# Optimization experiments

Measured on AMD Instinct MI355X. Metric: run time of the kernel, lower is better.

## Reference

```python
import jax, jax.numpy as jnp
import numpy as np

N_NODES = 50000

def gcn_conv(x, W, b, src, dst, n):
    # PyG GCNConv: h = x @ W; add self-loops; sym-normalized mean aggregation; + bias
    h = x @ W  # [N, out]
    deg = jax.ops.segment_sum(jnp.ones(src.shape[0], x.dtype), dst, num_segments=n) + 1.0  # +1 self-loop
    dinv = jax.lax.rsqrt(deg)  # deg^{-1/2}
    norm = dinv[src] * dinv[dst]  # [E]
    msg = h[src] * norm[:, None]  # [E, out]
    agg = jax.ops.segment_sum(msg, dst, num_segments=n)
    agg = agg + h * (dinv * dinv)[:, None]  # self-loop contribution, norm = 1/deg
    return agg + b


def setup_inputs() -> dict:
    key = jax.random.key(0)
    ks = jax.random.split(key, 12)
    f1, h1, h2, a = 128, 128, 64, N_NODES
    def glorot(k, shape):
        lim = float(np.sqrt(6.0 / (shape[0] + shape[1])))
        return jax.random.uniform(k, shape, jnp.float32, -lim, lim)
    x = jax.random.normal(ks[0], (N_NODES, f1), jnp.float32)
    edge_index = jax.random.randint(ks[1], (2, 800000), 0, N_NODES, dtype=jnp.int64)
    W1 = glorot(ks[2], (f1, h1)); b1 = jnp.zeros((h1,), jnp.float32)
    W2 = glorot(ks[3], (h1, h2)); b2 = jnp.zeros((h2,), jnp.float32)
    W3 = glorot(ks[4], (h2, 1));  b3 = jnp.zeros((1,), jnp.float32)
    lim4 = float(1.0 / np.sqrt(a))
    W4 = jax.random.uniform(ks[5], (a,), jnp.float32, -lim4, lim4)
    b4 = jax.random.uniform(ks[6], (1,), jnp.float32, -lim4, lim4)
    return {"x": x, "edge_index": edge_index, "W1": W1, "b1": b1,
            "W2": W2, "b2": b2, "W3": W3, "b3": b3, "W4": W4, "b4": b4}


def reference(x, edge_index, W1, b1, W2, b2, W3, b3, W4, b4):
    src, dst = edge_index[0], edge_index[1]
    n = x.shape[0]
    h = jnp.tanh(gcn_conv(x, W1, b1, src, dst, n))
    h = jnp.tanh(gcn_conv(h, W2, b2, src, dst, n))
    h = jnp.tanh(gcn_conv(h, W3, b3, src, dst, n))
    h = h.reshape(-1)  # [N] == action_dim
    out = jnp.dot(W4, h) + b4  # Linear(action_dim, 1) -> [1]
    return out
```

## Files before the change

kernel.cpp:

```cpp
#include <hip/hip_runtime.h>
#include <hip/hip_fp16.h>
#include <math.h>


constexpr int BLOCK = 256;
constexpr int SLOTS = 64;

__device__ inline unsigned int pack_h2(float a, float b) {
    __half2 h = __floats2half2_rn(a, b);
    return *reinterpret_cast<unsigned int*>(&h);
}
__device__ inline float2 unpack_h2(unsigned int u) {
    __half2 h = *reinterpret_cast<__half2*>(&u);
    return __half22float2(h);
}

template<int K, int M>
__global__ void __launch_bounds__(256) gemm1_fill(const float* __restrict__ X,
                                                  const float* __restrict__ W,
                                                  __half* __restrict__ H, int N, int ngemm,
                                                  const int* __restrict__ src,
                                                  const int* __restrict__ dst,
                                                  int* __restrict__ deg,
                                                  unsigned short* __restrict__ slots,
                                                  int E, int nfill) {
    __shared__ float xs[64][64];
    const int rem = blockIdx.x % 3;
    if (rem != 0) {
        int blk = (blockIdx.x / 3) * 2 + (rem - 1);
        if (blk >= nfill) return;
        int base = (blk * blockDim.x + threadIdx.x) * 2;
        if (base + 2 <= E) {
            int2 da = *reinterpret_cast<const int2*>(dst + base);
            int2 sa = *reinterpret_cast<const int2*>(src + base);
            int p0 = atomicAdd(&deg[da.x], 1);
            int p1 = atomicAdd(&deg[da.y], 1);
            if (p0 < SLOTS) slots[(size_t)da.x * SLOTS + p0] = (unsigned short)sa.x;
            if (p1 < SLOTS) slots[(size_t)da.y * SLOTS + p1] = (unsigned short)sa.y;
        } else {
            for (int e = base; e < E; ++e) {
                int d = dst[e];
                int p = atomicAdd(&deg[d], 1);
                if (p < SLOTS) slots[(size_t)d * SLOTS + p] = (unsigned short)src[e];
            }
        }
        return;
    }
    constexpr int BM = 64;
    constexpr int TN = 4;
    constexpr int TX = M / TN;
    constexpr int TY = 256 / TX;
    constexpr int TM = BM / TY;
    constexpr int KH4 = 16;

    int gblk = blockIdx.x / 3;
    if (gblk >= ngemm) return;
    const int tid = threadIdx.x;
    const int n0 = gblk * BM;

    if (gblk == 0 && tid < 32)
        reinterpret_cast<uint2*>(H + (size_t)N * M)[tid] = make_uint2(0u, 0u);

    const int tx = tid % TX;
    const int ty = tid / TX;
    const int col0 = tx * TN;
    const int row0 = ty * TM;

    float acc[TM][TN];
#pragma unroll
    for (int r = 0; r < TM; ++r)
#pragma unroll
        for (int c = 0; c < TN; ++c) acc[r][c] = 0.0f;

    const float4* X4 = reinterpret_cast<const float4*>(X);
    const float4* W4 = reinterpret_cast<const float4*>(W);
    constexpr int X4_PER_ROW = K / 4;
    constexpr int W4_PER_ROW = M / 4;

#pragma unroll
    for (int ph = 0; ph < 2; ++ph) {
#pragma unroll
        for (int i = 0; i < 4; ++i) {
            int idx = tid + i * 256;
            int row = idx >> 4;
            int k4 = idx & 15;
            float4 v = make_float4(0.f, 0.f, 0.f, 0.f);
            if (n0 + row < N) v = X4[(size_t)(n0 + row) * X4_PER_ROW + ph * KH4 + k4];
            *reinterpret_cast<float4*>(&xs[row][k4 * 4]) = v;
        }
        __syncthreads();
#pragma unroll 4
        for (int k4 = 0; k4 < KH4; ++k4) {
            int k4g = ph * KH4 + k4;
            float4 wv[4];
#pragma unroll
            for (int i = 0; i < 4; ++i)
                wv[i] = W4[(size_t)(k4g * 4 + i) * W4_PER_ROW + tx];
            float4 xv[TM];
#pragma unroll
            for (int r = 0; r < TM; ++r)
                xv[r] = *reinterpret_cast<const float4*>(&xs[row0 + r][k4 * 4]);
#pragma unroll
            for (int r = 0; r < TM; ++r) {
#pragma unroll
                for (int c = 0; c < TN; ++c) {
                    acc[r][c] = fmaf(xv[r].x, ((float*)&wv[0])[c], acc[r][c]);
                    acc[r][c] = fmaf(xv[r].y, ((float*)&wv[1])[c], acc[r][c]);
                    acc[r][c] = fmaf(xv[r].z, ((float*)&wv[2])[c], acc[r][c]);
                    acc[r][c] = fmaf(xv[r].w, ((float*)&wv[3])[c], acc[r][c]);
                }
            }
        }
        __syncthreads();
    }

#pragma unroll
    for (int r = 0; r < TM; ++r) {
        int row = n0 + row0 + r;
        if (row < N) {
            uint2 o;
            o.x = pack_h2(acc[r][0], acc[r][1]);
            o.y = pack_h2(acc[r][2], acc[r][3]);
            *reinterpret_cast<uint2*>(&H[(size_t)row * M + col0]) = o;
        }
    }
}

__global__ void dinv_scale(const int* __restrict__ deg, int* __restrict__ cnt,
                           float* __restrict__ dinv, uint2* __restrict__ Hh, int N) {
    int idx = blockIdx.x * blockDim.x + threadIdx.x;
    int n = idx >> 5, q = idx & 31;
    if (n > N) return;
    if (n == N) { if (q == 0) dinv[N] = 0.0f; return; }
    int dg = deg[n];
    float di = 1.0f / sqrtf((float)dg + 1.0f);
    if (q == 0) { dinv[n] = di; cnt[n] = min(dg, SLOTS); }
    uint2 u = Hh[idx];
    float2 a = unpack_h2(u.x);
    float2 b = unpack_h2(u.y);
    uint2 o;
    o.x = pack_h2(a.x * di, a.y * di);
    o.y = pack_h2(b.x * di, b.y * di);
    Hh[idx] = o;
}

template<int K, int M>
__global__ void __launch_bounds__(256) gemm_tiled(const float* __restrict__ X,
                                                  const float* __restrict__ W,
                                                  const float* __restrict__ dinv,
                                                  __half* __restrict__ H, int N) {
    constexpr int BM = 64;
    constexpr int TN = 4;
    constexpr int TX = M / TN;
    constexpr int TY = 256 / TX;
    constexpr int TM = BM / TY;
    constexpr int K4 = K / 4;

    __shared__ float xs[BM][K];

    const int tid = threadIdx.x;
    const int n0 = blockIdx.x * BM;

    if (blockIdx.x == 0 && tid < 16)
        reinterpret_cast<uint2*>(H + (size_t)N * M)[tid] = make_uint2(0u, 0u);

    {
        const float4* X4 = reinterpret_cast<const float4*>(X);
        constexpr int F4_PER_ROW = K / 4;
        constexpr int TOT = BM * F4_PER_ROW;
#pragma unroll
        for (int i = 0; i < TOT / 256; ++i) {
            int idx = tid + i * 256;
            int row = idx / F4_PER_ROW;
            int k4 = idx % F4_PER_ROW;
            float4 v = make_float4(0.f, 0.f, 0.f, 0.f);
            if (n0 + row < N) v = X4[(size_t)(n0 + row) * F4_PER_ROW + k4];
            *reinterpret_cast<float4*>(&xs[row][k4 * 4]) = v;
        }
    }
    __syncthreads();

    const int tx = tid % TX;
    const int ty = tid / TX;
    const int col0 = tx * TN;
    const int row0 = ty * TM;

    float acc[TM][TN];
#pragma unroll
    for (int r = 0; r < TM; ++r)
#pragma unroll
        for (int c = 0; c < TN; ++c) acc[r][c] = 0.0f;

    const float4* W4 = reinterpret_cast<const float4*>(W);
    constexpr int W4_PER_ROW = M / 4;

#pragma unroll 4
    for (int k4 = 0; k4 < K4; ++k4) {
        float4 wv[4];
#pragma unroll
        for (int i = 0; i < 4; ++i)
            wv[i] = W4[(size_t)(k4 * 4 + i) * W4_PER_ROW + tx];
        float4 xv[TM];
#pragma unroll
        for (int r = 0; r < TM; ++r)
            xv[r] = *reinterpret_cast<const float4*>(&xs[row0 + r][k4 * 4]);
#pragma unroll
        for (int r = 0; r < TM; ++r) {
#pragma unroll
            for (int c = 0; c < TN; ++c) {
                acc[r][c] = fmaf(xv[r].x, ((float*)&wv[0])[c], acc[r][c]);
                acc[r][c] = fmaf(xv[r].y, ((float*)&wv[1])[c], acc[r][c]);
                acc[r][c] = fmaf(xv[r].z, ((float*)&wv[2])[c], acc[r][c]);
                acc[r][c] = fmaf(xv[r].w, ((float*)&wv[3])[c], acc[r][c]);
            }
        }
    }

#pragma unroll
    for (int r = 0; r < TM; ++r) {
        int row = n0 + row0 + r;
        if (row < N) {
            float di = dinv[row];
            uint2 o;
            o.x = pack_h2(acc[r][0] * di, acc[r][1] * di);
            o.y = pack_h2(acc[r][2] * di, acc[r][3] * di);
            *reinterpret_cast<uint2*>(&H[(size_t)row * M + col0]) = o;
        }
    }
}

__global__ void __launch_bounds__(256) agg128(const int* __restrict__ cntA,
                                              const unsigned short* __restrict__ slots,
                                              const float* __restrict__ dinv,
                                              const __half* __restrict__ Hs,
                                              const float* __restrict__ bias,
                                              float* __restrict__ A, int N) {
    int wid = threadIdx.x >> 6;
    int lane = threadIdx.x & 63;
    int n = blockIdx.x * 4 + wid;
    if (n >= N) return;
    int half = lane >> 5, sub = lane & 31;
    const uint2* H2 = reinterpret_cast<const uint2*>(Hs);
    float4 acc = make_float4(0.f, 0.f, 0.f, 0.f);
    if (half == 0) {
        uint2 u = H2[(size_t)n * 32 + sub];
        float2 a = unpack_h2(u.x), b = unpack_h2(u.y);
        acc.x = a.x; acc.y = a.y; acc.z = b.x; acc.w = b.y;
    }
    int cnt = cntA[n];
    int idxv = (lane < cnt) ? (int)slots[(size_t)n * SLOTS + lane] : N;
    int cnt16 = (cnt + 15) & ~15;
    for (int j = 0; j < cnt16; j += 16) {
        int s0 = __shfl(idxv, j + half);
        int s1 = __shfl(idxv, j + 2 + half);
        int s2 = __shfl(idxv, j + 4 + half);
        int s3 = __shfl(idxv, j + 6 + half);
        int s4 = __shfl(idxv, j + 8 + half);
        int s5 = __shfl(idxv, j + 10 + half);
        int s6 = __shfl(idxv, j + 12 + half);
        int s7 = __shfl(idxv, j + 14 + half);
        uint2 u0 = H2[(size_t)s0 * 32 + sub];
        uint2 u1 = H2[(size_t)s1 * 32 + sub];
        uint2 u2 = H2[(size_t)s2 * 32 + sub];
        uint2 u3 = H2[(size_t)s3 * 32 + sub];
        uint2 u4 = H2[(size_t)s4 * 32 + sub];
        uint2 u5 = H2[(size_t)s5 * 32 + sub];
        uint2 u6 = H2[(size_t)s6 * 32 + sub];
        uint2 u7 = H2[(size_t)s7 * 32 + sub];
        float2 a0 = unpack_h2(u0.x), b0 = unpack_h2(u0.y);
        float2 a1 = unpack_h2(u1.x), b1 = unpack_h2(u1.y);
        float2 a2 = unpack_h2(u2.x), b2 = unpack_h2(u2.y);
        float2 a3 = unpack_h2(u3.x), b3 = unpack_h2(u3.y);
        float2 a4 = unpack_h2(u4.x), b4 = unpack_h2(u4.y);
        float2 a5 = unpack_h2(u5.x), b5 = unpack_h2(u5.y);
        float2 a6 = unpack_h2(u6.x), b6 = unpack_h2(u6.y);
        float2 a7 = unpack_h2(u7.x), b7 = unpack_h2(u7.y);
        acc.x += (a0.x + a1.x) + (a2.x + a3.x) + (a4.x + a5.x) + (a6.x + a7.x);
        acc.y += (a0.y + a1.y) + (a2.y + a3.y) + (a4.y + a5.y) + (a6.y + a7.y);
        acc.z += (b0.x + b1.x) + (b2.x + b3.x) + (b4.x + b5.x) + (b6.x + b7.x);
        acc.w += (b0.y + b1.y) + (b2.y + b3.y) + (b4.y + b5.y) + (b6.y + b7.y);
    }
    acc.x += __shfl_down(acc.x, 32);
    acc.y += __shfl_down(acc.y, 32);
    acc.z += __shfl_down(acc.z, 32);
    acc.w += __shfl_down(acc.w, 32);
    if (half == 0) {
        float di = dinv[n];
        float4 b = reinterpret_cast<const float4*>(bias)[sub];
        float4 o;
        o.x = tanhf(acc.x * di + b.x);
        o.y = tanhf(acc.y * di + b.y);
        o.z = tanhf(acc.z * di + b.z);
        o.w = tanhf(acc.w * di + b.w);
        reinterpret_cast<float4*>(A)[(size_t)n * 32 + sub] = o;
    }
}

__global__ void __launch_bounds__(256) agg64_dot3(const int* __restrict__ cntA,
                                                  const unsigned short* __restrict__ slots,
                                                  const float* __restrict__ dinv,
                                                  const __half* __restrict__ Hs,
                                                  const float* __restrict__ b2,
                                                  const float* __restrict__ W3,
                                                  float* __restrict__ Hs3, int N) {
    int wid = threadIdx.x >> 6;
    int lane = threadIdx.x & 63;
    int n = blockIdx.x * 4 + wid;
    if (n >= N) return;
    int grp = lane >> 4, sub = lane & 15;
    const uint2* H2 = reinterpret_cast<const uint2*>(Hs);
    float4 acc = make_float4(0.f, 0.f, 0.f, 0.f);
    if (grp == 0) {
        uint2 u = H2[(size_t)n * 16 + sub];
        float2 a = unpack_h2(u.x), b = unpack_h2(u.y);
        acc.x = a.x; acc.y = a.y; acc.z = b.x; acc.w = b.y;
    }
    int cnt = cntA[n];
    int idxv = (lane < cnt) ? (int)slots[(size_t)n * SLOTS + lane] : N;
    int cnt16 = (cnt + 15) & ~15;
    int j = 0;
    for (; j + 32 <= cnt16; j += 32) {
        int s0 = __shfl(idxv, j + grp);
        int s1 = __shfl(idxv, j + 4 + grp);
        int s2 = __shfl(idxv, j + 8 + grp);
        int s3 = __shfl(idxv, j + 12 + grp);
        int s4 = __shfl(idxv, j + 16 + grp);
        int s5 = __shfl(idxv, j + 20 + grp);
        int s6 = __shfl(idxv, j + 24 + grp);
        int s7 = __shfl(idxv, j + 28 + grp);
        uint2 u0 = H2[(size_t)s0 * 16 + sub];
        uint2 u1 = H2[(size_t)s1 * 16 + sub];
        uint2 u2 = H2[(size_t)s2 * 16 + sub];
        uint2 u3 = H2[(size_t)s3 * 16 + sub];
        uint2 u4 = H2[(size_t)s4 * 16 + sub];
        uint2 u5 = H2[(size_t)s5 * 16 + sub];
        uint2 u6 = H2[(size_t)s6 * 16 + sub];
        uint2 u7 = H2[(size_t)s7 * 16 + sub];
        float2 a0 = unpack_h2(u0.x), b0 = unpack_h2(u0.y);
        float2 a1 = unpack_h2(u1.x), b1 = unpack_h2(u1.y);
        float2 a2 = unpack_h2(u2.x), b2f = unpack_h2(u2.y);
        float2 a3 = unpack_h2(u3.x), b3f = unpack_h2(u3.y);
        float2 a4 = unpack_h2(u4.x), b4f = unpack_h2(u4.y);
        float2 a5 = unpack_h2(u5.x), b5f = unpack_h2(u5.y);
        float2 a6 = unpack_h2(u6.x), b6f = unpack_h2(u6.y);
        float2 a7 = unpack_h2(u7.x), b7f = unpack_h2(u7.y);
        acc.x += (a0.x + a1.x) + (a2.x + a3.x) + (a4.x + a5.x) + (a6.x + a7.x);
        acc.y += (a0.y + a1.y) + (a2.y + a3.y) + (a4.y + a5.y) + (a6.y + a7.y);
        acc.z += (b0.x + b1.x) + (b2f.x + b3f.x) + (b4f.x + b5f.x) + (b6f.x + b7f.x);
        acc.w += (b0.y + b1.y) + (b2f.y + b3f.y) + (b4f.y + b5f.y) + (b6f.y + b7f.y);
    }
    for (; j < cnt16; j += 16) {
        int s0 = __shfl(idxv, j + grp);
        int s1 = __shfl(idxv, j + 4 + grp);
        int s2 = __shfl(idxv, j + 8 + grp);
        int s3 = __shfl(idxv, j + 12 + grp);
        uint2 u0 = H2[(size_t)s0 * 16 + sub];
        uint2 u1 = H2[(size_t)s1 * 16 + sub];
        uint2 u2 = H2[(size_t)s2 * 16 + sub];
        uint2 u3 = H2[(size_t)s3 * 16 + sub];
        float2 a0 = unpack_h2(u0.x), b0 = unpack_h2(u0.y);
        float2 a1 = unpack_h2(u1.x), b1 = unpack_h2(u1.y);
        float2 a2 = unpack_h2(u2.x), b2f = unpack_h2(u2.y);
        float2 a3 = unpack_h2(u3.x), b3f = unpack_h2(u3.y);
        acc.x += (a0.x + a1.x) + (a2.x + a3.x);
        acc.y += (a0.y + a1.y) + (a2.y + a3.y);
        acc.z += (b0.x + b1.x) + (b2f.x + b3f.x);
        acc.w += (b0.y + b1.y) + (b2f.y + b3f.y);
    }
    acc.x += __shfl_xor(acc.x, 16);
    acc.y += __shfl_xor(acc.y, 16);
    acc.z += __shfl_xor(acc.z, 16);
    acc.w += __shfl_xor(acc.w, 16);
    acc.x += __shfl_xor(acc.x, 32);
    acc.y += __shfl_xor(acc.y, 32);
    acc.z += __shfl_xor(acc.z, 32);
    acc.w += __shfl_xor(acc.w, 32);
    float di = dinv[n];
    float4 b = reinterpret_cast<const float4*>(b2)[sub];
    float4 w = reinterpret_cast<const float4*>(W3)[sub];
    float t = tanhf(acc.x * di + b.x) * w.x
            + tanhf(acc.y * di + b.y) * w.y
            + tanhf(acc.z * di + b.z) * w.z
            + tanhf(acc.w * di + b.w) * w.w;
#pragma unroll
    for (int off = 1; off < 16; off <<= 1) t += __shfl_xor(t, off);
    if (lane == 0) Hs3[n] = t * di;
}

__global__ void __launch_bounds__(256) agg_dot(const int* __restrict__ cntA,
                                               const unsigned short* __restrict__ slots,
                                               const float* __restrict__ dinv,
                                               const float* __restrict__ Hs,
                                               const float* __restrict__ b3,
                                               const float* __restrict__ W4,
                                               float* __restrict__ partials, int N) {
    __shared__ float sm[4];
    int wid = threadIdx.x >> 6;
    int lane = threadIdx.x & 63;
    int n = blockIdx.x * 4 + wid;
    float p = 0.0f;
    if (n < N) {
        int cnt = cntA[n];
        float acc = (lane < cnt) ? Hs[(int)slots[(size_t)n * SLOTS + lane]] : 0.0f;
#pragma unroll
        for (int off = 32; off > 0; off >>= 1) acc += __shfl_down(acc, off);
        if (lane == 0) {
            float h = tanhf((acc + Hs[n]) * dinv[n] + b3[0]);
            p = W4[n] * h;
        }
    }
    if (lane == 0) sm[wid] = p;
    __syncthreads();
    if (threadIdx.x == 0) partials[blockIdx.x] = sm[0] + sm[1] + sm[2] + sm[3];
}

__global__ void final_sum(const float* __restrict__ partials, int B,
                          const float* __restrict__ b4, float* __restrict__ out) {
    float acc = 0.0f;
    for (int i = threadIdx.x; i < B; i += blockDim.x) acc += partials[i];
#pragma unroll
    for (int off = 32; off > 0; off >>= 1) acc += __shfl_down(acc, off);
    __shared__ float sm[4];
    int lane = threadIdx.x & 63, wid = threadIdx.x >> 6;
    if (lane == 0) sm[wid] = acc;
    __syncthreads();
    if (threadIdx.x == 0) out[0] = sm[0] + sm[1] + sm[2] + sm[3] + b4[0];
}

extern "C" void kernel_launch(void* const* d_in, const int* in_sizes, int n_in,
                              void* d_out, int out_size, void* d_ws, size_t ws_size,
                              hipStream_t stream) {
    const float* x  = (const float*)d_in[0];
    const int*   ei = (const int*)d_in[1];
    const float* W1 = (const float*)d_in[2];
    const float* b1 = (const float*)d_in[3];
    const float* W2 = (const float*)d_in[4];
    const float* b2 = (const float*)d_in[5];
    const float* W3 = (const float*)d_in[6];
    const float* b3 = (const float*)d_in[7];
    const float* W4 = (const float*)d_in[8];
    const float* b4 = (const float*)d_in[9];

    const int N = in_sizes[0] / 128;
    const int E = in_sizes[1] / 2;
    const int* src = ei;
    const int* dst = ei + E;

    const int nblkW = (N + 3) / 4;

    float* base = (float*)d_ws;
    size_t off = 0;
    auto alloc = [&](size_t cnt, size_t align_f) -> float* {
        off = (off + align_f - 1) / align_f * align_f;
        float* p = base + off;
        off += cnt;
        return p;
    };
    int* deg     = (int*)alloc(N, 1);
    int* cnt     = (int*)alloc(N, 1);
    float* dinv  = alloc(N + 1, 1);
    unsigned short* slots = (unsigned short*)alloc((size_t)N * SLOTS / 2, 64);
    __half* H1h  = (__half*)alloc((size_t)(N + 1) * 64, 64);
    float* bufB  = alloc((size_t)N * 128, 64);
    float* partials = alloc(nblkW, 64);

    __half* hs2 = H1h;

    const int ngemm = (N + 63) / 64;
    const int nfill = (E + 511) / 512;
    const int fhalf = (nfill + 1) / 2;
    const int nfused = 3 * ((ngemm > fhalf) ? ngemm : fhalf);
    const int nscale = (N * 32 + 32 + BLOCK - 1) / BLOCK;

    hipMemsetAsync(deg, 0, (size_t)N * sizeof(int), stream);
    gemm1_fill<128, 128><<<nfused, 256, 0, stream>>>(x, W1, H1h, N, ngemm,
                                                     src, dst, deg, slots, E, nfill);
    dinv_scale<<<nscale, BLOCK, 0, stream>>>(deg, cnt, dinv, (uint2*)H1h, N);

    agg128<<<nblkW, 256, 0, stream>>>(cnt, slots, dinv, H1h, b1, bufB, N);

    gemm_tiled<128, 64><<<ngemm, 256, 0, stream>>>(bufB, W2, dinv, hs2, N);
    agg64_dot3<<<nblkW, 256, 0, stream>>>(cnt, slots, dinv, hs2, b2, W3, bufB, N);

    agg_dot<<<nblkW, 256, 0, stream>>>(cnt, slots, dinv, bufB, b3, W4, partials, N);
    final_sum<<<1, BLOCK, 0, stream>>>(partials, nblkW, b4, (float*)d_out);
}
```

Before: 247.5 us.

## Build slot lists via bucketed two-pass scatter instead of global atomics

Replaces the per-edge global atomic slot fill with a coarse bucket sort. A histogram kernel counts edges per 256-node bucket and a scan computes bucket offsets. The fused GEMM kernel then scatters packed (dst,src) keys into bucket order, and a per-bucket group kernel builds degrees and slot lists with shared-memory atomics. The goal is to cut contended random global atomics and scattered writes, at the cost of three extra launches and an extra pass over the edges. The packing relies on node ids fitting in 16 bits, which the 50000-node input satisfies.

```diff
diff --git a/kernel.cpp b/kernel.cpp
--- a/kernel.cpp
+++ b/kernel.cpp
@@ -15,33 +15,84 @@
     return __half22float2(h);
 }
 
+__global__ void __launch_bounds__(256) hist_kernel(const int* __restrict__ dst,
+                                                   int* __restrict__ gh, int E) {
+    __shared__ int lh[256];
+    int tid = threadIdx.x;
+    lh[tid] = 0;
+    __syncthreads();
+#pragma unroll
+    for (int j = 0; j < 4; ++j) {
+        int e = blockIdx.x * 1024 + tid + j * 256;
+        if (e < E) atomicAdd(&lh[dst[e] >> 8], 1);
+    }
+    __syncthreads();
+    if (lh[tid] > 0) atomicAdd(&gh[tid], lh[tid]);
+}
+
+__global__ void __launch_bounds__(256) scan_kernel(const int* __restrict__ gh,
+                                                   int* __restrict__ base,
+                                                   int* __restrict__ gcur,
+                                                   int NB, int E) {
+    __shared__ int s[256];
+    int tid = threadIdx.x;
+    int v = (tid < NB) ? gh[tid] : 0;
+    s[tid] = v;
+    __syncthreads();
+    for (int off = 1; off < 256; off <<= 1) {
+        int x = s[tid];
+        if (tid >= off) x += s[tid - off];
+        __syncthreads();
+        s[tid] = x;
+        __syncthreads();
+    }
+    if (tid < NB) {
+        int excl = s[tid] - v;
+        base[tid] = excl;
+        gcur[tid] = excl;
+    }
+    if (tid == 0) base[NB] = E;
+}
+
 template<int K, int M>
-__global__ void __launch_bounds__(256) gemm1_fill(const float* __restrict__ X,
+__global__ void __launch_bounds__(256) gemm1_scat(const float* __restrict__ X,
                                                   const float* __restrict__ W,
                                                   __half* __restrict__ H, int N, int ngemm,
                                                   const int* __restrict__ src,
                                                   const int* __restrict__ dst,
-                                                  int* __restrict__ deg,
-                                                  unsigned short* __restrict__ slots,
-                                                  int E, int nfill) {
+                                                  int* __restrict__ gcur,
+                                                  unsigned int* __restrict__ ebuf,
+                                                  int E, int nscat) {
     __shared__ float xs[64][64];
-    const int rem = blockIdx.x % 3;
-    if (rem != 0) {
-        int blk = (blockIdx.x / 3) * 2 + (rem - 1);
-        if (blk >= nfill) return;
-        int base = (blk * blockDim.x + threadIdx.x) * 2;
-        if (base + 2 <= E) {
-            int2 da = *reinterpret_cast<const int2*>(dst + base);
-            int2 sa = *reinterpret_cast<const int2*>(src + base);
-            int p0 = atomicAdd(&deg[da.x], 1);
-            int p1 = atomicAdd(&deg[da.y], 1);
-            if (p0 < SLOTS) slots[(size_t)da.x * SLOTS + p0] = (unsigned short)sa.x;
-            if (p1 < SLOTS) slots[(size_t)da.y * SLOTS + p1] = (unsigned short)sa.y;
-        } else {
-            for (int e = base; e < E; ++e) {
-                int d = dst[e];
-                int p = atomicAdd(&deg[d], 1);
-                if (p < SLOTS) slots[(size_t)d * SLOTS + p] = (unsigned short)src[e];
+    const int tid = threadIdx.x;
+    if (blockIdx.x & 1) {
+        int blk = blockIdx.x >> 1;
+        if (blk >= nscat) return;
+        int* lh = (int*)&xs[0][0];
+        int* gb = lh + 256;
+        lh[tid] = 0;
+        __syncthreads();
+        int ev[4], dv[4], lr[4];
+        bool val[4];
+#pragma unroll
+        for (int j = 0; j < 4; ++j) {
+            int e = blk * 1024 + tid + j * 256;
+            val[j] = (e < E);
+            ev[j] = e;
+            if (val[j]) {
+                dv[j] = dst[e];
+                lr[j] = atomicAdd(&lh[dv[j] >> 8], 1);
+            }
+        }
+        __syncthreads();
+        if (lh[tid] > 0) gb[tid] = atomicAdd(&gcur[tid], lh[tid]);
+        __syncthreads();
+#pragma unroll
+        for (int j = 0; j < 4; ++j) {
+            if (val[j]) {
+                int pos = gb[dv[j] >> 8] + lr[j];
+                ebuf[pos] = ((unsigned int)dv[j] << 16) |
+                            ((unsigned int)src[ev[j]] & 0xFFFFu);
             }
         }
         return;
@@ -53,9 +104,8 @@
     constexpr int TM = BM / TY;
     constexpr int KH4 = 16;
 
-    int gblk = blockIdx.x / 3;
+    int gblk = blockIdx.x >> 1;
     if (gblk >= ngemm) return;
-    const int tid = threadIdx.x;
     const int n0 = gblk * BM;
 
     if (gblk == 0 && tid < 32)
@@ -123,6 +173,35 @@
             o.y = pack_h2(acc[r][2], acc[r][3]);
             *reinterpret_cast<uint2*>(&H[(size_t)row * M + col0]) = o;
         }
+    }
+}
+
+__global__ void __launch_bounds__(256) group_kernel(const unsigned int* __restrict__ ebuf,
+                                                    const int* __restrict__ base,
+                                                    int* __restrict__ deg,
+                                                    unsigned short* __restrict__ slots,
+                                                    int N) {
+    __shared__ int cnt[256];
+    __shared__ int cur[256];
+    int tid = threadIdx.x;
+    int b = blockIdx.x;
+    cnt[tid] = 0;
+    cur[tid] = 0;
+    __syncthreads();
+    int lo = base[b], hi = base[b + 1];
+    for (int i = lo + tid; i < hi; i += 256) {
+        unsigned int key = ebuf[i];
+        atomicAdd(&cnt[(key >> 16) & 255u], 1);
+    }
+    __syncthreads();
+    int d0 = (b << 8) + tid;
+    if (d0 < N) deg[d0] = cnt[tid];
+    for (int i = lo + tid; i < hi; i += 256) {
+        unsigned int key = ebuf[i];
+        unsigned int d = key >> 16;
+        int p = atomicAdd(&cur[d & 255u], 1);
+        if (p < SLOTS)
+            slots[(size_t)d * SLOTS + p] = (unsigned short)(key & 0xFFFFu);
     }
 }
 
@@ -447,18 +526,23 @@
     const int* dst = ei + E;
 
     const int nblkW = (N + 3) / 4;
-
-    float* base = (float*)d_ws;
+    const int NB = (N + 255) >> 8;
+
+    float* base_ws = (float*)d_ws;
     size_t off = 0;
     auto alloc = [&](size_t cnt, size_t align_f) -> float* {
         off = (off + align_f - 1) / align_f * align_f;
-        float* p = base + off;
+        float* p = base_ws + off;
         off += cnt;
         return p;
     };
     int* deg     = (int*)alloc(N, 1);
     int* cnt     = (int*)alloc(N, 1);
     float* dinv  = alloc(N + 1, 1);
+    int* gh      = (int*)alloc(256, 64);
+    int* bbase   = (int*)alloc(260, 64);
+    int* gcur    = (int*)alloc(256, 64);
+    unsigned int* ebuf = (unsigned int*)alloc(E, 64);
     unsigned short* slots = (unsigned short*)alloc((size_t)N * SLOTS / 2, 64);
     __half* H1h  = (__half*)alloc((size_t)(N + 1) * 64, 64);
     float* bufB  = alloc((size_t)N * 128, 64);
@@ -467,14 +551,17 @@
     __half* hs2 = H1h;
 
     const int ngemm = (N + 63) / 64;
-    const int nfill = (E + 511) / 512;
-    const int fhalf = (nfill + 1) / 2;
-    const int nfused = 3 * ((ngemm > fhalf) ? ngemm : fhalf);
+    const int nscat = (E + 1023) / 1024;
+    const int nmax  = (ngemm > nscat) ? ngemm : nscat;
     const int nscale = (N * 32 + 32 + BLOCK - 1) / BLOCK;
 
-    hipMemsetAsync(deg, 0, (size_t)N * sizeof(int), stream);
-    gemm1_fill<128, 128><<<nfused, 256, 0, stream>>>(x, W1, H1h, N, ngemm,
-                                                     src, dst, deg, slots, E, nfill);
+    hipMemsetAsync(gh, 0, 256 * sizeof(int), stream);
+    hist_kernel<<<nscat, 256, 0, stream>>>(dst, gh, E);
+    scan_kernel<<<1, 256, 0, stream>>>(gh, bbase, gcur, NB, E);
+    gemm1_scat<128, 128><<<2 * nmax, 256, 0, stream>>>(x, W1, H1h, N, ngemm,
+                                                       src, dst, gcur, ebuf, E, nscat);
+    group_kernel<<<NB, 256, 0, stream>>>(ebuf, bbase, deg, slots, N);
+
     dinv_scale<<<nscale, BLOCK, 0, stream>>>(deg, cnt, dinv, (uint2*)H1h, N);
 
     agg128<<<nblkW, 256, 0, stream>>>(cnt, slots, dinv, H1h, b1, bufB, N);
```

Result: slower. 273.0 us (+10.3%).

## Drop dinv_scale and final_sum kernels; recompute deg^-1/2 inline and fuse final reduction

Applied to the files above, without the earlier changes.

Removes the separate dinv_scale pass that rescaled H1 and stored dinv/cnt. Each consumer now computes rsqrt(deg+1) on the fly, and agg128 applies the source-node normalization per neighbor through an extra gathered deg load and shuffle. The final_sum launch is folded into agg_dot with a last-block-done atomic ticket. This saves two launches and a full read-write pass over H1, at the cost of an extra random gather of deg per edge in agg128 plus extra multiplies. The padding index N reads deg[N], which the memset zeroes, but that is harmless since the padded H row is zero.

```diff
diff --git a/kernel.cpp b/kernel.cpp
--- a/kernel.cpp
+++ b/kernel.cpp
@@ -126,112 +126,8 @@
     }
 }
 
-__global__ void dinv_scale(const int* __restrict__ deg, int* __restrict__ cnt,
-                           float* __restrict__ dinv, uint2* __restrict__ Hh, int N) {
-    int idx = blockIdx.x * blockDim.x + threadIdx.x;
-    int n = idx >> 5, q = idx & 31;
-    if (n > N) return;
-    if (n == N) { if (q == 0) dinv[N] = 0.0f; return; }
-    int dg = deg[n];
-    float di = 1.0f / sqrtf((float)dg + 1.0f);
-    if (q == 0) { dinv[n] = di; cnt[n] = min(dg, SLOTS); }
-    uint2 u = Hh[idx];
-    float2 a = unpack_h2(u.x);
-    float2 b = unpack_h2(u.y);
-    uint2 o;
-    o.x = pack_h2(a.x * di, a.y * di);
-    o.y = pack_h2(b.x * di, b.y * di);
-    Hh[idx] = o;
-}
-
-template<int K, int M>
-__global__ void __launch_bounds__(256) gemm_tiled(const float* __restrict__ X,
-                                                  const float* __restrict__ W,
-                                                  const float* __restrict__ dinv,
-                                                  __half* __restrict__ H, int N) {
-    constexpr int BM = 64;
-    constexpr int TN = 4;
-    constexpr int TX = M / TN;
-    constexpr int TY = 256 / TX;
-    constexpr int TM = BM / TY;
-    constexpr int K4 = K / 4;
-
-    __shared__ float xs[BM][K];
-
-    const int tid = threadIdx.x;
-    const int n0 = blockIdx.x * BM;
-
-    if (blockIdx.x == 0 && tid < 16)
-        reinterpret_cast<uint2*>(H + (size_t)N * M)[tid] = make_uint2(0u, 0u);
-
-    {
-        const float4* X4 = reinterpret_cast<const float4*>(X);
-        constexpr int F4_PER_ROW = K / 4;
-        constexpr int TOT = BM * F4_PER_ROW;
-#pragma unroll
-        for (int i = 0; i < TOT / 256; ++i) {
-            int idx = tid + i * 256;
-            int row = idx / F4_PER_ROW;
-            int k4 = idx % F4_PER_ROW;
-            float4 v = make_float4(0.f, 0.f, 0.f, 0.f);
-            if (n0 + row < N) v = X4[(size_t)(n0 + row) * F4_PER_ROW + k4];
-            *reinterpret_cast<float4*>(&xs[row][k4 * 4]) = v;
-        }
-    }
-    __syncthreads();
-
-    const int tx = tid % TX;
-    const int ty = tid / TX;
-    const int col0 = tx * TN;
-    const int row0 = ty * TM;
-
-    float acc[TM][TN];
-#pragma unroll
-    for (int r = 0; r < TM; ++r)
-#pragma unroll
-        for (int c = 0; c < TN; ++c) acc[r][c] = 0.0f;
-
-    const float4* W4 = reinterpret_cast<const float4*>(W);
-    constexpr int W4_PER_ROW = M / 4;
-
-#pragma unroll 4
-    for (int k4 = 0; k4 < K4; ++k4) {
-        float4 wv[4];
-#pragma unroll
-        for (int i = 0; i < 4; ++i)
-            wv[i] = W4[(size_t)(k4 * 4 + i) * W4_PER_ROW + tx];
-        float4 xv[TM];
-#pragma unroll
-        for (int r = 0; r < TM; ++r)
-            xv[r] = *reinterpret_cast<const float4*>(&xs[row0 + r][k4 * 4]);
-#pragma unroll
-        for (int r = 0; r < TM; ++r) {
-#pragma unroll
-            for (int c = 0; c < TN; ++c) {
-                acc[r][c] = fmaf(xv[r].x, ((float*)&wv[0])[c], acc[r][c]);
-                acc[r][c] = fmaf(xv[r].y, ((float*)&wv[1])[c], acc[r][c]);
-                acc[r][c] = fmaf(xv[r].z, ((float*)&wv[2])[c], acc[r][c]);
-                acc[r][c] = fmaf(xv[r].w, ((float*)&wv[3])[c], acc[r][c]);
-            }
-        }
-    }
-
-#pragma unroll
-    for (int r = 0; r < TM; ++r) {
-        int row = n0 + row0 + r;
-        if (row < N) {
-            float di = dinv[row];
-            uint2 o;
-            o.x = pack_h2(acc[r][0] * di, acc[r][1] * di);
-            o.y = pack_h2(acc[r][2] * di, acc[r][3] * di);
-            *reinterpret_cast<uint2*>(&H[(size_t)row * M + col0]) = o;
-        }
-    }
-}
-
-__global__ void __launch_bounds__(256) agg128(const int* __restrict__ cntA,
+__global__ void __launch_bounds__(256) agg128(const int* __restrict__ deg,
                                               const unsigned short* __restrict__ slots,
-                                              const float* __restrict__ dinv,
                                               const __half* __restrict__ Hs,
                                               const float* __restrict__ bias,
                                               float* __restrict__ A, int N) {
@@ -241,24 +137,32 @@
     if (n >= N) return;
     int half = lane >> 5, sub = lane & 31;
     const uint2* H2 = reinterpret_cast<const uint2*>(Hs);
+    int dg = deg[n];
+    int cnt = min(dg, SLOTS);
+    float din = rsqrtf((float)dg + 1.0f);
     float4 acc = make_float4(0.f, 0.f, 0.f, 0.f);
     if (half == 0) {
         uint2 u = H2[(size_t)n * 32 + sub];
         float2 a = unpack_h2(u.x), b = unpack_h2(u.y);
-        acc.x = a.x; acc.y = a.y; acc.z = b.x; acc.w = b.y;
-    }
-    int cnt = cntA[n];
-    int idxv = (lane < cnt) ? (int)slots[(size_t)n * SLOTS + lane] : N;
+        acc.x = a.x * din; acc.y = a.y * din;
+        acc.z = b.x * din; acc.w = b.y * din;
+    }
+    int idxv = N;
+    float dvv = 0.0f;
+    if (lane < cnt) {
+        idxv = (int)slots[(size_t)n * SLOTS + lane];
+        dvv = rsqrtf((float)deg[idxv] + 1.0f);
+    }
     int cnt16 = (cnt + 15) & ~15;
     for (int j = 0; j < cnt16; j += 16) {
-        int s0 = __shfl(idxv, j + half);
-        int s1 = __shfl(idxv, j + 2 + half);
-        int s2 = __shfl(idxv, j + 4 + half);
-        int s3 = __shfl(idxv, j + 6 + half);
-        int s4 = __shfl(idxv, j + 8 + half);
-        int s5 = __shfl(idxv, j + 10 + half);
-        int s6 = __shfl(idxv, j + 12 + half);
-        int s7 = __shfl(idxv, j + 14 + half);
+        int s0 = __shfl(idxv, j + half);       float d0 = __shfl(dvv, j + half);
+        int s1 = __shfl(idxv, j + 2 + half);   float d1 = __shfl(dvv, j + 2 + half);
+        int s2 = __shfl(idxv, j + 4 + half);   float d2 = __shfl(dvv, j + 4 + half);
+        int s3 = __shfl(idxv, j + 6 + half);   float d3 = __shfl(dvv, j + 6 + half);
+        int s4 = __shfl(idxv, j + 8 + half);   float d4 = __shfl(dvv, j + 8 + half);
+        int s5 = __shfl(idxv, j + 10 + half);  float d5 = __shfl(dvv, j + 10 + half);
+        int s6 = __shfl(idxv, j + 12 + half);  float d6 = __shfl(dvv, j + 12 + half);
+        int s7 = __shfl(idxv, j + 14 + half);  float d7 = __shfl(dvv, j + 14 + half);
         uint2 u0 = H2[(size_t)s0 * 32 + sub];
         uint2 u1 = H2[(size_t)s1 * 32 + sub];
         uint2 u2 = H2[(size_t)s2 * 32 + sub];
@@ -275,30 +179,117 @@
         float2 a5 = unpack_h2(u5.x), b5 = unpack_h2(u5.y);
         float2 a6 = unpack_h2(u6.x), b6 = unpack_h2(u6.y);
         float2 a7 = unpack_h2(u7.x), b7 = unpack_h2(u7.y);
-        acc.x += (a0.x + a1.x) + (a2.x + a3.x) + (a4.x + a5.x) + (a6.x + a7.x);
-        acc.y += (a0.y + a1.y) + (a2.y + a3.y) + (a4.y + a5.y) + (a6.y + a7.y);
-        acc.z += (b0.x + b1.x) + (b2.x + b3.x) + (b4.x + b5.x) + (b6.x + b7.x);
-        acc.w += (b0.y + b1.y) + (b2.y + b3.y) + (b4.y + b5.y) + (b6.y + b7.y);
+        acc.x += (a0.x * d0 + a1.x * d1) + (a2.x * d2 + a3.x * d3)
+               + (a4.x * d4 + a5.x * d5) + (a6.x * d6 + a7.x * d7);
+        acc.y += (a0.y * d0 + a1.y * d1) + (a2.y * d2 + a3.y * d3)
+               + (a4.y * d4 + a5.y * d5) + (a6.y * d6 + a7.y * d7);
+        acc.z += (b0.x * d0 + b1.x * d1) + (b2.x * d2 + b3.x * d3)
+               + (b4.x * d4 + b5.x * d5) + (b6.x * d6 + b7.x * d7);
+        acc.w += (b0.y * d0 + b1.y * d1) + (b2.y * d2 + b3.y * d3)
+               + (b4.y * d4 + b5.y * d5) + (b6.y * d6 + b7.y * d7);
     }
     acc.x += __shfl_down(acc.x, 32);
     acc.y += __shfl_down(acc.y, 32);
     acc.z += __shfl_down(acc.z, 32);
     acc.w += __shfl_down(acc.w, 32);
     if (half == 0) {
-        float di = dinv[n];
         float4 b = reinterpret_cast<const float4*>(bias)[sub];
         float4 o;
-        o.x = tanhf(acc.x * di + b.x);
-        o.y = tanhf(acc.y * di + b.y);
-        o.z = tanhf(acc.z * di + b.z);
-        o.w = tanhf(acc.w * di + b.w);
+        o.x = tanhf(acc.x * din + b.x);
+        o.y = tanhf(acc.y * din + b.y);
+        o.z = tanhf(acc.z * din + b.z);
+        o.w = tanhf(acc.w * din + b.w);
         reinterpret_cast<float4*>(A)[(size_t)n * 32 + sub] = o;
     }
 }
 
-__global__ void __launch_bounds__(256) agg64_dot3(const int* __restrict__ cntA,
+template<int K, int M>
+__global__ void __launch_bounds__(256) gemm_tiled(const float* __restrict__ X,
+                                                  const float* __restrict__ W,
+                                                  const int* __restrict__ deg,
+                                                  __half* __restrict__ H, int N) {
+    constexpr int BM = 64;
+    constexpr int TN = 4;
+    constexpr int TX = M / TN;
+    constexpr int TY = 256 / TX;
+    constexpr int TM = BM / TY;
+    constexpr int K4 = K / 4;
+
+    __shared__ float xs[BM][K];
+
+    const int tid = threadIdx.x;
+    const int n0 = blockIdx.x * BM;
+
+    if (blockIdx.x == 0 && tid < 16)
+        reinterpret_cast<uint2*>(H + (size_t)N * M)[tid] = make_uint2(0u, 0u);
+
+    {
+        const float4* X4 = reinterpret_cast<const float4*>(X);
+        constexpr int F4_PER_ROW = K / 4;
+        constexpr int TOT = BM * F4_PER_ROW;
+#pragma unroll
+        for (int i = 0; i < TOT / 256; ++i) {
+            int idx = tid + i * 256;
+            int row = idx / F4_PER_ROW;
+            int k4 = idx % F4_PER_ROW;
+            float4 v = make_float4(0.f, 0.f, 0.f, 0.f);
+            if (n0 + row < N) v = X4[(size_t)(n0 + row) * F4_PER_ROW + k4];
+            *reinterpret_cast<float4*>(&xs[row][k4 * 4]) = v;
+        }
+    }
+    __syncthreads();
+
+    const int tx = tid % TX;
+    const int ty = tid / TX;
+    const int col0 = tx * TN;
+    const int row0 = ty * TM;
+
+    float acc[TM][TN];
+#pragma unroll
+    for (int r = 0; r < TM; ++r)
+#pragma unroll
+        for (int c = 0; c < TN; ++c) acc[r][c] = 0.0f;
+
+    const float4* W4 = reinterpret_cast<const float4*>(W);
+    constexpr int W4_PER_ROW = M / 4;
+
+#pragma unroll 4
+    for (int k4 = 0; k4 < K4; ++k4) {
+        float4 wv[4];
+#pragma unroll
+        for (int i = 0; i < 4; ++i)
+            wv[i] = W4[(size_t)(k4 * 4 + i) * W4_PER_ROW + tx];
+        float4 xv[TM];
+#pragma unroll
+        for (int r = 0; r < TM; ++r)
+            xv[r] = *reinterpret_cast<const float4*>(&xs[row0 + r][k4 * 4]);
+#pragma unroll
+        for (int r = 0; r < TM; ++r) {
+#pragma unroll
+            for (int c = 0; c < TN; ++c) {
+                acc[r][c] = fmaf(xv[r].x, ((float*)&wv[0])[c], acc[r][c]);
+                acc[r][c] = fmaf(xv[r].y, ((float*)&wv[1])[c], acc[r][c]);
+                acc[r][c] = fmaf(xv[r].z, ((float*)&wv[2])[c], acc[r][c]);
+                acc[r][c] = fmaf(xv[r].w, ((float*)&wv[3])[c], acc[r][c]);
+            }
+        }
+    }
+
+#pragma unroll
+    for (int r = 0; r < TM; ++r) {
+        int row = n0 + row0 + r;
+        if (row < N) {
+            float di = rsqrtf((float)deg[row] + 1.0f);
+            uint2 o;
+            o.x = pack_h2(acc[r][0] * di, acc[r][1] * di);
+            o.y = pack_h2(acc[r][2] * di, acc[r][3] * di);
+            *reinterpret_cast<uint2*>(&H[(size_t)row * M + col0]) = o;
+        }
+    }
+}
+
+__global__ void __launch_bounds__(256) agg64_dot3(const int* __restrict__ deg,
                                                   const unsigned short* __restrict__ slots,
-                                                  const float* __restrict__ dinv,
                                                   const __half* __restrict__ Hs,
                                                   const float* __restrict__ b2,
                                                   const float* __restrict__ W3,
@@ -309,13 +300,14 @@
     if (n >= N) return;
     int grp = lane >> 4, sub = lane & 15;
     const uint2* H2 = reinterpret_cast<const uint2*>(Hs);
+    int dg = deg[n];
+    int cnt = min(dg, SLOTS);
     float4 acc = make_float4(0.f, 0.f, 0.f, 0.f);
     if (grp == 0) {
         uint2 u = H2[(size_t)n * 16 + sub];
         float2 a = unpack_h2(u.x), b = unpack_h2(u.y);
         acc.x = a.x; acc.y = a.y; acc.z = b.x; acc.w = b.y;
     }
-    int cnt = cntA[n];
     int idxv = (lane < cnt) ? (int)slots[(size_t)n * SLOTS + lane] : N;
     int cnt16 = (cnt + 15) & ~15;
     int j = 0;
@@ -375,7 +367,7 @@
     acc.y += __shfl_xor(acc.y, 32);
     acc.z += __shfl_xor(acc.z, 32);
     acc.w += __shfl_xor(acc.w, 32);
-    float di = dinv[n];
+    float di = rsqrtf((float)dg + 1.0f);
     float4 b = reinterpret_cast<const float4*>(b2)[sub];
     float4 w = reinterpret_cast<const float4*>(W3)[sub];
     float t = tanhf(acc.x * di + b.x) * w.x
@@ -387,44 +379,51 @@
     if (lane == 0) Hs3[n] = t * di;
 }
 
-__global__ void __launch_bounds__(256) agg_dot(const int* __restrict__ cntA,
+__global__ void __launch_bounds__(256) agg_dot(const int* __restrict__ deg,
                                                const unsigned short* __restrict__ slots,
-                                               const float* __restrict__ dinv,
                                                const float* __restrict__ Hs,
                                                const float* __restrict__ b3,
                                                const float* __restrict__ W4,
-                                               float* __restrict__ partials, int N) {
+                                               float* __restrict__ partials,
+                                               const float* __restrict__ b4,
+                                               int* __restrict__ done,
+                                               float* __restrict__ out, int N, int B) {
     __shared__ float sm[4];
+    __shared__ unsigned int ticket;
     int wid = threadIdx.x >> 6;
     int lane = threadIdx.x & 63;
     int n = blockIdx.x * 4 + wid;
     float p = 0.0f;
     if (n < N) {
-        int cnt = cntA[n];
+        int dg = deg[n];
+        int cnt = min(dg, SLOTS);
         float acc = (lane < cnt) ? Hs[(int)slots[(size_t)n * SLOTS + lane]] : 0.0f;
 #pragma unroll
         for (int off = 32; off > 0; off >>= 1) acc += __shfl_down(acc, off);
         if (lane == 0) {
-            float h = tanhf((acc + Hs[n]) * dinv[n] + b3[0]);
+            float di = rsqrtf((float)dg + 1.0f);
+            float h = tanhf((acc + Hs[n]) * di + b3[0]);
             p = W4[n] * h;
         }
     }
     if (lane == 0) sm[wid] = p;
     __syncthreads();
-    if (threadIdx.x == 0) partials[blockIdx.x] = sm[0] + sm[1] + sm[2] + sm[3];
-}
-
-__global__ void final_sum(const float* __restrict__ partials, int B,
-                          const float* __restrict__ b4, float* __restrict__ out) {
-    float acc = 0.0f;
-    for (int i = threadIdx.x; i < B; i += blockDim.x) acc += partials[i];
-#pragma unroll
-    for (int off = 32; off > 0; off >>= 1) acc += __shfl_down(acc, off);
-    __shared__ float sm[4];
-    int lane = threadIdx.x & 63, wid = threadIdx.x >> 6;
-    if (lane == 0) sm[wid] = acc;
+    if (threadIdx.x == 0) {
+        partials[blockIdx.x] = sm[0] + sm[1] + sm[2] + sm[3];
+        __threadfence();
+        ticket = (unsigned int)atomicAdd(done, 1);
+    }
     __syncthreads();
-    if (threadIdx.x == 0) out[0] = sm[0] + sm[1] + sm[2] + sm[3] + b4[0];
+    if (ticket == (unsigned int)(gridDim.x - 1)) {
+        __threadfence();
+        float acc2 = 0.0f;
+        for (int i = threadIdx.x; i < B; i += 256) acc2 += partials[i];
+#pragma unroll
+        for (int off = 32; off > 0; off >>= 1) acc2 += __shfl_down(acc2, off);
+        if (lane == 0) sm[wid] = acc2;
+        __syncthreads();
+        if (threadIdx.x == 0) out[0] = sm[0] + sm[1] + sm[2] + sm[3] + b4[0];
+    }
 }
 
 extern "C" void kernel_launch(void* const* d_in, const int* in_sizes, int n_in,
@@ -456,32 +455,29 @@
         off += cnt;
         return p;
     };
-    int* deg     = (int*)alloc(N, 1);
-    int* cnt     = (int*)alloc(N, 1);
-    float* dinv  = alloc(N + 1, 1);
+    int* deg     = (int*)alloc(N + 2, 1);
     unsigned short* slots = (unsigned short*)alloc((size_t)N * SLOTS / 2, 64);
     __half* H1h  = (__half*)alloc((size_t)(N + 1) * 64, 64);
     float* bufB  = alloc((size_t)N * 128, 64);
     float* partials = alloc(nblkW, 64);
 
+    int* done = deg + N + 1;
     __half* hs2 = H1h;
 
     const int ngemm = (N + 63) / 64;
     const int nfill = (E + 511) / 512;
     const int fhalf = (nfill + 1) / 2;
     const int nfused = 3 * ((ngemm > fhalf) ? ngemm : fhalf);
-    const int nscale = (N * 32 + 32 + BLOCK - 1) / BLOCK;
-
-    hipMemsetAsync(deg, 0, (size_t)N * sizeof(int), stream);
+
+    hipMemsetAsync(deg, 0, (size_t)(N + 2) * sizeof(int), stream);
     gemm1_fill<128, 128><<<nfused, 256, 0, stream>>>(x, W1, H1h, N, ngemm,
                                                      src, dst, deg, slots, E, nfill);
-    dinv_scale<<<nscale, BLOCK, 0, stream>>>(deg, cnt, dinv, (uint2*)H1h, N);
-
-    agg128<<<nblkW, 256, 0, stream>>>(cnt, slots, dinv, H1h, b1, bufB, N);
-
-    gemm_tiled<128, 64><<<ngemm, 256, 0, stream>>>(bufB, W2, dinv, hs2, N);
-    agg64_dot3<<<nblkW, 256, 0, stream>>>(cnt, slots, dinv, hs2, b2, W3, bufB, N);
-
-    agg_dot<<<nblkW, 256, 0, stream>>>(cnt, slots, dinv, bufB, b3, W4, partials, N);
-    final_sum<<<1, BLOCK, 0, stream>>>(partials, nblkW, b4, (float*)d_out);
-}
+
+    agg128<<<nblkW, 256, 0, stream>>>(deg, slots, H1h, b1, bufB, N);
+
+    gemm_tiled<128, 64><<<ngemm, 256, 0, stream>>>(bufB, W2, deg, hs2, N);
+    agg64_dot3<<<nblkW, 256, 0, stream>>>(deg, slots, hs2, b2, W3, bufB, N);
+
+    agg_dot<<<nblkW, 256, 0, stream>>>(deg, slots, bufB, b3, W4, partials,
+                                       b4, done, (float*)d_out, N, nblkW);
+}
```

After: 465.6 us. +88.1%, slower.
